# Performance work log

Measured on AMD Instinct MI355X. Metric: run time of the kernel, lower is better.

## Reference

```python
import jax, jax.numpy as jnp
import numpy as np

B, T, D, H, E = 4, 2048, 1024, 2048, 8
TOP_K = int(E * 0.25)  # = 2


def setup_inputs() -> dict:
    key = jax.random.key(0)
    ks = jax.random.split(key, 6)
    x = jax.random.normal(ks[0], (B, T, D), dtype=jnp.float32)
    gate = jax.random.normal(ks[1], (D, E), dtype=jnp.float32)
    # per-expert 2-layer MLP params (D -> H -> D), stacked over experts
    W1 = jax.random.normal(ks[2], (E, D, H), dtype=jnp.float32) * (D ** -0.5)
    b1 = jnp.zeros((E, H), dtype=jnp.float32)
    W2 = jax.random.normal(ks[3], (E, H, D), dtype=jnp.float32) * (H ** -0.5)
    b2 = jnp.zeros((E, D), dtype=jnp.float32)
    return {"x": x, "gate": gate, "W1": W1, "b1": b1, "W2": W2, "b2": b2}


def reference(x, gate, W1, b1, W2, b2):
    # gating: softmax over experts, then top-k mask, renormalize (L1 over experts)
    raw_gate = jax.nn.softmax(jnp.einsum('btd,de->bte', x, gate), axis=-1)  # [B,T,E]
    topk_scores, topk_idx = jax.lax.top_k(raw_gate, TOP_K)                   # [B,T,k]
    mask = jax.nn.one_hot(topk_idx, E, dtype=raw_gate.dtype).sum(axis=-2)    # [B,T,E]
    gate_topk = mask * raw_gate
    gate_topk = gate_topk / jnp.maximum(gate_topk.sum(axis=-1, keepdims=True), 1e-12)
    # dense all-expert compute (faithful to the original: every expert sees every token)
    h = jax.nn.relu(jnp.einsum('btd,edh->beth', x, W1) + b1[None, :, None, :])  # [B,E,T,H]
    expert_out = jnp.einsum('beth,ehd->betd', h, W2) + b2[None, :, None, :]     # [B,E,T,D]
    # weighted combine
    out = jnp.einsum('bte,betd->btd', gate_topk, expert_out)  # [B,T,D]
    return out
```

## Files before the change

### kernel.cpp

```cpp
#include <hip/hip_runtime.h>

#define E_      8
#define D_      1024
#define H_      2048
#define TOKENS  8192
#define RROWS   16384
#define HPAD_ROWS (RROWS + 128)

using bf16x8 = __attribute__((ext_vector_type(8))) __bf16;
using f32x4  = __attribute__((ext_vector_type(4))) float;

__device__ __forceinline__ unsigned short f2bf(float f) {
  unsigned u = __builtin_bit_cast(unsigned, f);
  u += 0x7fffu + ((u >> 16) & 1u);
  return (unsigned short)(u >> 16);
}
__device__ __forceinline__ float bf2f(unsigned short u) {
  unsigned v = (unsigned)u << 16;
  return __builtin_bit_cast(float, v);
}

#define GLDS16(g, l) __builtin_amdgcn_global_load_lds( \
    (const __attribute__((address_space(1))) unsigned int*)(g), \
    (__attribute__((address_space(3))) unsigned int*)(l), 16, 0, 0)

#define SBAR() asm volatile("s_barrier" ::: "memory")


__global__ void transpose_cvt2_kernel(const float* __restrict__ W1,
                                      unsigned short* __restrict__ w1t,
                                      const float* __restrict__ W2,
                                      unsigned short* __restrict__ w2t) {
  int b = blockIdx.x;
  const int nb1 = E_ * (D_ >> 6) * (H_ >> 6);
  const float* src; unsigned short* dst; int R, C;
  if (b < nb1) { src = W1; dst = w1t; R = D_; C = H_; }
  else         { src = W2; dst = w2t; R = H_; C = D_; b -= nb1; }
  int tilesC = C >> 6;
  int per = (R >> 6) * tilesC;
  int e = b / per, rem = b % per;
  int rb = rem / tilesC, cb = rem % tilesC;
  __shared__ float tile[64][65];
  const float* s = src + (size_t)e * R * C;
  unsigned short* d = dst + (size_t)e * R * C;
  int r0 = rb << 6, c0 = cb << 6;
#pragma unroll
  for (int i = 0; i < 16; i++) {
    int idx = threadIdx.x + i * 256;
    int lr = idx >> 6, lc = idx & 63;
    tile[lr][lc] = s[(size_t)(r0 + lr) * C + (c0 + lc)];
  }
  __syncthreads();
#pragma unroll
  for (int i = 0; i < 16; i++) {
    int idx = threadIdx.x + i * 256;
    int lr = idx >> 6, lc = idx & 63;
    d[(size_t)(c0 + lr) * R + (r0 + lc)] = f2bf(tile[lc][lr]);
  }
}

__global__ void gating_kernel(const float* __restrict__ x, const float* __restrict__ gate,
                              unsigned short* __restrict__ xb,
                              int* __restrict__ sel, float* __restrict__ wsel) {
  int lane = threadIdx.x & 63, wid = threadIdx.x >> 6;
  int t = (blockIdx.x << 2) + wid;
  const float* xr = x + (size_t)t * D_;
  unsigned short* xbr = xb + (size_t)t * D_;
  float acc[8];
#pragma unroll
  for (int e = 0; e < 8; e++) acc[e] = 0.f;
#pragma unroll
  for (int i = 0; i < 4; i++) {
    int d0 = (i << 8) + (lane << 2);
    float4 xv = *reinterpret_cast<const float4*>(xr + d0);
    ushort4 o = make_ushort4(f2bf(xv.x), f2bf(xv.y), f2bf(xv.z), f2bf(xv.w));
    *reinterpret_cast<ushort4*>(xbr + d0) = o;
    float xa[4] = {xv.x, xv.y, xv.z, xv.w};
#pragma unroll
    for (int j = 0; j < 4; j++) {
      const float4* g4 = reinterpret_cast<const float4*>(gate + (size_t)(d0 + j) * 8);
      float4 ga = g4[0], gb = g4[1];
      acc[0] += xa[j] * ga.x; acc[1] += xa[j] * ga.y;
      acc[2] += xa[j] * ga.z; acc[3] += xa[j] * ga.w;
      acc[4] += xa[j] * gb.x; acc[5] += xa[j] * gb.y;
      acc[6] += xa[j] * gb.z; acc[7] += xa[j] * gb.w;
    }
  }
#pragma unroll
  for (int e = 0; e < 8; e++) {
#pragma unroll
    for (int off = 32; off; off >>= 1) acc[e] += __shfl_xor(acc[e], off);
  }
  if (lane == 0) {
    int i0 = 0; float v0 = acc[0];
#pragma unroll
    for (int e = 1; e < 8; e++) if (acc[e] > v0) { v0 = acc[e]; i0 = e; }
    int i1 = -1; float v1 = -3.4e38f;
#pragma unroll
    for (int e = 0; e < 8; e++) if (e != i0 && acc[e] > v1) { v1 = acc[e]; i1 = e; }
    float p1 = expf(v1 - v0);
    float inv = 1.f / (1.f + p1);
    sel[t * 2] = i0; sel[t * 2 + 1] = i1;
    wsel[t * 2] = inv; wsel[t * 2 + 1] = p1 * inv;
  }
}

__global__ __launch_bounds__(1024) void route_kernel(
    const int* __restrict__ sel, int* __restrict__ cnt, int* __restrict__ off,
    int* __restrict__ tok_id, int* __restrict__ pos) {
  const int tid = threadIdx.x;
  const int lane = tid & 63, wid = tid >> 6;
  __shared__ int wtot[16][8];
  __shared__ int woff[16][8];
  __shared__ int offs[8];
  int sv[16];
  const int s0 = tid << 4;
#pragma unroll
  for (int q = 0; q < 4; q++) {
    int4 v = reinterpret_cast<const int4*>(sel + s0)[q];
    sv[q * 4 + 0] = v.x; sv[q * 4 + 1] = v.y;
    sv[q * 4 + 2] = v.z; sv[q * 4 + 3] = v.w;
  }
  int h[8];
#pragma unroll
  for (int e = 0; e < 8; e++) h[e] = 0;
#pragma unroll
  for (int j = 0; j < 16; j++) {
    int ev = sv[j];
#pragma unroll
    for (int e = 0; e < 8; e++) h[e] += (ev == e) ? 1 : 0;
  }
  int excl[8];
#pragma unroll
  for (int e = 0; e < 8; e++) {
    int v = h[e];
#pragma unroll
    for (int d = 1; d < 64; d <<= 1) {
      int u = __shfl_up(v, d);
      if (lane >= d) v += u;
    }
    excl[e] = v - h[e];
    if (lane == 63) wtot[wid][e] = v;
  }
  __syncthreads();
  if (tid == 0) {
    int run[8];
#pragma unroll
    for (int e = 0; e < 8; e++) run[e] = 0;
    for (int w = 0; w < 16; w++)
#pragma unroll
      for (int e = 0; e < 8; e++) { woff[w][e] = run[e]; run[e] += wtot[w][e]; }
    int a = 0;
    for (int e = 0; e < 8; e++) { offs[e] = a; off[e] = a; cnt[e] = run[e]; a += run[e]; }
  }
  __syncthreads();
  int base[8];
#pragma unroll
  for (int e = 0; e < 8; e++) base[e] = offs[e] + woff[wid][e] + excl[e];
#pragma unroll
  for (int j = 0; j < 16; j++) {
    int ev = sv[j];
    int p = 0;
#pragma unroll
    for (int e = 0; e < 8; e++) if (ev == e) { p = base[e]; base[e] = p + 1; }
    pos[s0 + j] = p;
    tok_id[p] = (s0 + j) >> 1;
  }
}


#define STAGE_A(slot, kh) do { \
  const size_t ko = (size_t)(kh) << 7; \
  _Pragma("unroll") \
  for (int i = 0; i < 4; i++) \
    GLDS16(Ab + gA[i] + ko, &Asm[slot][((wid << 2) + i) << 9]); \
} while (0)
#define STAGE_B(slot, kh) do { \
  const size_t ko = (size_t)(kh) << 7; \
  _Pragma("unroll") \
  for (int i = 0; i < 4; i++) \
    GLDS16(Bb + gB[i] + ko, &Bsm[slot][((wid << 2) + i) << 9]); \
} while (0)

__global__ __launch_bounds__(256, 2) void gemm1_kernel(
    const unsigned short* __restrict__ xb,
    const unsigned short* __restrict__ w1t,
    const float* __restrict__ b1,
    unsigned short* __restrict__ hbuf,
    const int* __restrict__ tok_id,
    const int* __restrict__ cnt, const int* __restrict__ off) {
  const int nwg = E_ * 64 * 16;
  const int raw = blockIdx.x;
  const int bid = (raw & 7) * (nwg >> 3) + (raw >> 3);
  const int e  = bid >> 10;
  const int rb = (bid >> 4) & 63;
  const int cb = bid & 15;
  const int rows = cnt[e];
  const int m0 = rb << 7;
  if (m0 >= rows) return;
  const int base = off[e];
  const int tid = threadIdx.x, lane = tid & 63, wid = tid >> 6;
  const int wr = wid >> 1, wc = wid & 1;

  __shared__ __align__(16) unsigned short Asm[2][128 * 64];
  __shared__ __align__(16) unsigned short Bsm[2][128 * 64];

  const int c8 = lane & 7, r8 = lane >> 3;
  const size_t swz = (size_t)((c8 ^ r8) << 4);
  size_t gA[4], gB[4];
  const int n0 = cb << 7;
#pragma unroll
  for (int i = 0; i < 4; i++) {
    int r = ((wid << 2) + i) << 3;
    int ar = m0 + r + r8; if (ar >= rows) ar = rows - 1;
    gA[i] = (size_t)tok_id[base + ar] * (D_ * 2) + swz;
    gB[i] = (size_t)(n0 + r + r8) * (D_ * 2) + swz;
  }
  const char* Ab = (const char*)xb;
  const char* Bb = (const char*)w1t + (size_t)e * H_ * D_ * 2;

  const int aRow = ((wr << 6) + (lane & 15)) * 128;
  const int bRow = ((wc << 6) + (lane & 15)) * 128;
  const int cby0 = (((lane >> 4)) ^ (lane & 7)) << 4;
  const int cby1 = ((4 + (lane >> 4)) ^ (lane & 7)) << 4;

  f32x4 acc[4][4] = {};
  const int KH = D_ / 64;

  STAGE_A(0, 0); STAGE_B(0, 0);
  STAGE_A(1, 1); STAGE_B(1, 1);
  asm volatile("s_waitcnt vmcnt(8)" ::: "memory");
  SBAR();

  for (int kh = 0; kh < KH; ++kh) {
    const int cur = kh & 1;
    const char* Ap = (const char*)&Asm[cur][0] + aRow;
    const char* Bp = (const char*)&Bsm[cur][0] + bRow;
    bf16x8 a[4], b[4], a2[4], b2[4];
#pragma unroll
    for (int m = 0; m < 4; m++) a[m]  = *(const bf16x8*)(Ap + cby0 + m * 2048);
#pragma unroll
    for (int n = 0; n < 4; n++) b[n]  = *(const bf16x8*)(Bp + cby0 + n * 2048);
#pragma unroll
    for (int m = 0; m < 4; m++) a2[m] = *(const bf16x8*)(Ap + cby1 + m * 2048);
#pragma unroll
    for (int n = 0; n < 4; n++) b2[n] = *(const bf16x8*)(Bp + cby1 + n * 2048);
    asm volatile("s_waitcnt lgkmcnt(0)" ::: "memory");
    __builtin_amdgcn_sched_barrier(0);
    SBAR();
    if (kh + 2 < KH) STAGE_A(cur, kh + 2);
    __builtin_amdgcn_s_setprio(1);
#pragma unroll
    for (int m = 0; m < 4; m++)
#pragma unroll
      for (int n = 0; n < 4; n++)
        acc[m][n] = __builtin_amdgcn_mfma_f32_16x16x32_bf16(a[m], b[n], acc[m][n], 0, 0, 0);
    __builtin_amdgcn_s_setprio(0);
    if (kh + 2 < KH) STAGE_B(cur, kh + 2);
    __builtin_amdgcn_s_setprio(1);
#pragma unroll
    for (int m = 0; m < 4; m++)
#pragma unroll
      for (int n = 0; n < 4; n++)
        acc[m][n] = __builtin_amdgcn_mfma_f32_16x16x32_bf16(a2[m], b2[n], acc[m][n], 0, 0, 0);
    __builtin_amdgcn_s_setprio(0);
    if (kh + 2 < KH) {
      asm volatile("s_waitcnt vmcnt(8)" ::: "memory");
    } else if (kh + 1 < KH) {
      asm volatile("s_waitcnt vmcnt(0)" ::: "memory");
    }
    SBAR();
  }

  const int rcnt = rows - m0;
  const float* b1e = b1 + e * H_;
#pragma unroll
  for (int m = 0; m < 4; m++) {
#pragma unroll
    for (int q = 0; q < 4; q++) {
      int rl = (wr << 6) + (m << 4) + ((lane >> 4) << 2) + q;
      if (rl < rcnt) {
        unsigned short* hrow = hbuf + (size_t)(base + m0 + rl) * H_;
#pragma unroll
        for (int n = 0; n < 4; n++) {
          int ncol = n0 + (wc << 6) + (n << 4) + (lane & 15);
          float v = acc[m][n][q] + b1e[ncol];
          hrow[ncol] = f2bf(fmaxf(v, 0.f));
        }
      }
    }
  }
}

__global__ __launch_bounds__(256, 2) void gemm2_kernel(
    const unsigned short* __restrict__ hbuf,
    const unsigned short* __restrict__ w2t,
    unsigned short* __restrict__ eout,
    const int* __restrict__ cnt, const int* __restrict__ off) {
  const int nwg = E_ * 64 * 8;
  const int raw = blockIdx.x;
  const int bid = (raw & 7) * (nwg >> 3) + (raw >> 3);
  const int e  = bid >> 9;
  const int rb = (bid >> 3) & 63;
  const int cb = bid & 7;
  const int rows = cnt[e];
  const int m0 = rb << 7;
  if (m0 >= rows) return;
  const int base = off[e];
  const int tid = threadIdx.x, lane = tid & 63, wid = tid >> 6;
  const int wr = wid >> 1, wc = wid & 1;

  __shared__ __align__(16) unsigned short Asm[2][128 * 64];
  __shared__ __align__(16) unsigned short Bsm[2][128 * 64];

  const int c8 = lane & 7, r8 = lane >> 3;
  const size_t swz = (size_t)((c8 ^ r8) << 4);
  size_t gA[4], gB[4];
  const int n0 = cb << 7;
#pragma unroll
  for (int i = 0; i < 4; i++) {
    int r = ((wid << 2) + i) << 3;
    gA[i] = (size_t)(base + m0 + r + r8) * (H_ * 2) + swz;
    gB[i] = (size_t)(n0 + r + r8) * (H_ * 2) + swz;
  }
  const char* Ab = (const char*)hbuf;
  const char* Bb = (const char*)w2t + (size_t)e * D_ * H_ * 2;

  const int aRow = ((wr << 6) + (lane & 15)) * 128;
  const int bRow = ((wc << 6) + (lane & 15)) * 128;
  const int cby0 = (((lane >> 4)) ^ (lane & 7)) << 4;
  const int cby1 = ((4 + (lane >> 4)) ^ (lane & 7)) << 4;

  f32x4 acc[4][4] = {};
  const int KH = H_ / 64;

  STAGE_A(0, 0); STAGE_B(0, 0);
  STAGE_A(1, 1); STAGE_B(1, 1);
  asm volatile("s_waitcnt vmcnt(8)" ::: "memory");
  SBAR();

  for (int kh = 0; kh < KH; ++kh) {
    const int cur = kh & 1;
    const char* Ap = (const char*)&Asm[cur][0] + aRow;
    const char* Bp = (const char*)&Bsm[cur][0] + bRow;
    bf16x8 a[4], b[4], a2[4], b2[4];
#pragma unroll
    for (int m = 0; m < 4; m++) a[m]  = *(const bf16x8*)(Ap + cby0 + m * 2048);
#pragma unroll
    for (int n = 0; n < 4; n++) b[n]  = *(const bf16x8*)(Bp + cby0 + n * 2048);
#pragma unroll
    for (int m = 0; m < 4; m++) a2[m] = *(const bf16x8*)(Ap + cby1 + m * 2048);
#pragma unroll
    for (int n = 0; n < 4; n++) b2[n] = *(const bf16x8*)(Bp + cby1 + n * 2048);
    asm volatile("s_waitcnt lgkmcnt(0)" ::: "memory");
    __builtin_amdgcn_sched_barrier(0);
    SBAR();
    if (kh + 2 < KH) STAGE_A(cur, kh + 2);
    __builtin_amdgcn_s_setprio(1);
#pragma unroll
    for (int m = 0; m < 4; m++)
#pragma unroll
      for (int n = 0; n < 4; n++)
        acc[m][n] = __builtin_amdgcn_mfma_f32_16x16x32_bf16(a[m], b[n], acc[m][n], 0, 0, 0);
    __builtin_amdgcn_s_setprio(0);
    if (kh + 2 < KH) STAGE_B(cur, kh + 2);
    __builtin_amdgcn_s_setprio(1);
#pragma unroll
    for (int m = 0; m < 4; m++)
#pragma unroll
      for (int n = 0; n < 4; n++)
        acc[m][n] = __builtin_amdgcn_mfma_f32_16x16x32_bf16(a2[m], b2[n], acc[m][n], 0, 0, 0);
    __builtin_amdgcn_s_setprio(0);
    if (kh + 2 < KH) {
      asm volatile("s_waitcnt vmcnt(8)" ::: "memory");
    } else if (kh + 1 < KH) {
      asm volatile("s_waitcnt vmcnt(0)" ::: "memory");
    }
    SBAR();
  }

  const int rcnt = rows - m0;
#pragma unroll
  for (int m = 0; m < 4; m++) {
#pragma unroll
    for (int q = 0; q < 4; q++) {
      int rl = (wr << 6) + (m << 4) + ((lane >> 4) << 2) + q;
      if (rl < rcnt) {
        unsigned short* erow = eout + (size_t)(base + m0 + rl) * D_;
#pragma unroll
        for (int n = 0; n < 4; n++) {
          int ncol = n0 + (wc << 6) + (n << 4) + (lane & 15);
          erow[ncol] = f2bf(acc[m][n][q]);
        }
      }
    }
  }
}

__global__ void combine_kernel(const unsigned short* __restrict__ eout,
                               const float* __restrict__ b2,
                               const int* __restrict__ sel, const float* __restrict__ wsel,
                               const int* __restrict__ pos,
                               float* __restrict__ out) {
  int t = (blockIdx.x << 2) + (threadIdx.x >> 6);
  int lane = threadIdx.x & 63;
  int e0 = sel[t * 2], e1 = sel[t * 2 + 1];
  float w0 = wsel[t * 2], w1 = wsel[t * 2 + 1];
  int p0 = pos[t * 2], p1 = pos[t * 2 + 1];
  const unsigned short* y0r = eout + (size_t)p0 * D_;
  const unsigned short* y1r = eout + (size_t)p1 * D_;
  const float* c0r = b2 + (size_t)e0 * D_;
  const float* c1r = b2 + (size_t)e1 * D_;
  float* orow = out + (size_t)t * D_;
#pragma unroll
  for (int j = 0; j < 4; j++) {
    int d = (j << 8) + (lane << 2);
    ushort4 y0 = *reinterpret_cast<const ushort4*>(y0r + d);
    ushort4 y1 = *reinterpret_cast<const ushort4*>(y1r + d);
    float4 c0 = *reinterpret_cast<const float4*>(c0r + d);
    float4 c1 = *reinterpret_cast<const float4*>(c1r + d);
    float4 o;
    o.x = w0 * (bf2f(y0.x) + c0.x) + w1 * (bf2f(y1.x) + c1.x);
    o.y = w0 * (bf2f(y0.y) + c0.y) + w1 * (bf2f(y1.y) + c1.y);
    o.z = w0 * (bf2f(y0.z) + c0.z) + w1 * (bf2f(y1.z) + c1.z);
    o.w = w0 * (bf2f(y0.w) + c0.w) + w1 * (bf2f(y1.w) + c1.w);
    *reinterpret_cast<float4*>(orow + d) = o;
  }
}


extern "C" void kernel_launch(void* const* d_in, const int* in_sizes, int n_in,
                              void* d_out, int out_size, void* d_ws, size_t ws_size,
                              hipStream_t stream) {
  (void)in_sizes; (void)n_in; (void)ws_size; (void)out_size;
  const float* x    = (const float*)d_in[0];
  const float* gate = (const float*)d_in[1];
  const float* W1   = (const float*)d_in[2];
  const float* b1   = (const float*)d_in[3];
  const float* W2   = (const float*)d_in[4];
  const float* b2   = (const float*)d_in[5];
  float* out = (float*)d_out;

  char* p = (char*)d_ws;
  unsigned short* xb   = (unsigned short*)p; p += (size_t)TOKENS * D_ * 2;
  unsigned short* w1t  = (unsigned short*)p; p += (size_t)E_ * H_ * D_ * 2;
  unsigned short* w2t  = (unsigned short*)p; p += (size_t)E_ * D_ * H_ * 2;
  unsigned short* hbuf = (unsigned short*)p; p += (size_t)HPAD_ROWS * H_ * 2;
  int*   tok  = (int*)p;   p += (size_t)RROWS * 4;
  int*   pos  = (int*)p;   p += (size_t)TOKENS * 2 * 4;
  int*   sel  = (int*)p;   p += (size_t)TOKENS * 2 * 4;
  float* wsel = (float*)p; p += (size_t)TOKENS * 2 * 4;
  int* cnt    = (int*)p;   p += 32 * 4;
  int* off    = (int*)p;   p += 32 * 4;
  unsigned short* eout = w1t;

  const int nb1 = E_ * (D_ / 64) * (H_ / 64);
  const int nb2 = E_ * (H_ / 64) * (D_ / 64);
  transpose_cvt2_kernel<<<nb1 + nb2, 256, 0, stream>>>(W1, w1t, W2, w2t);
  gating_kernel<<<TOKENS / 4, 256, 0, stream>>>(x, gate, xb, sel, wsel);
  route_kernel<<<1, 1024, 0, stream>>>(sel, cnt, off, tok, pos);
  gemm1_kernel<<<E_ * 64 * 16, 256, 0, stream>>>(xb, w1t, b1, hbuf, tok, cnt, off);
  gemm2_kernel<<<E_ * 64 * 8, 256, 0, stream>>>(hbuf, w2t, eout, cnt, off);
  combine_kernel<<<TOKENS / 4, 256, 0, stream>>>(eout, b2, sel, wsel, pos, out);
}
```

Before: 295.1 us.

## Fuse gating into transpose prologue and widen gemm1 tile to 128x256 with 512 threads

Merges the gating kernel and the weight transpose/convert kernel into one launch, so one kernel boundary goes away and the two independent stages can run at the same time. Rewrites gemm1 to use 8 waves per workgroup, each block covering 128 rows by 256 columns of H. The wider tile means the gathered A rows are reused across twice as many columns. The cost is one workgroup per CU (launch bounds 512,1), which lowers occupancy, and the MFMA chains are merged without the interleaved B staging.

After: 297.1 us. No clear change (+0.7%).

```diff
diff --git a/kernel.cpp b/kernel.cpp
--- a/kernel.cpp
+++ b/kernel.cpp
@@ -27,11 +27,59 @@
 #define SBAR() asm volatile("s_barrier" ::: "memory")
 
 
-__global__ void transpose_cvt2_kernel(const float* __restrict__ W1,
-                                      unsigned short* __restrict__ w1t,
-                                      const float* __restrict__ W2,
-                                      unsigned short* __restrict__ w2t) {
+__global__ void prologue_kernel(const float* __restrict__ x, const float* __restrict__ gate,
+                                unsigned short* __restrict__ xb,
+                                int* __restrict__ sel, float* __restrict__ wsel,
+                                const float* __restrict__ W1, unsigned short* __restrict__ w1t,
+                                const float* __restrict__ W2, unsigned short* __restrict__ w2t) {
+  __shared__ float tile[64][65];
   int b = blockIdx.x;
+  const int NG = TOKENS / 4;
+  if (b < NG) {
+    int lane = threadIdx.x & 63, wid = threadIdx.x >> 6;
+    int t = (b << 2) + wid;
+    const float* xr = x + (size_t)t * D_;
+    unsigned short* xbr = xb + (size_t)t * D_;
+    float acc[8];
+#pragma unroll
+    for (int e = 0; e < 8; e++) acc[e] = 0.f;
+#pragma unroll
+    for (int i = 0; i < 4; i++) {
+      int d0 = (i << 8) + (lane << 2);
+      float4 xv = *reinterpret_cast<const float4*>(xr + d0);
+      ushort4 o = make_ushort4(f2bf(xv.x), f2bf(xv.y), f2bf(xv.z), f2bf(xv.w));
+      *reinterpret_cast<ushort4*>(xbr + d0) = o;
+      float xa[4] = {xv.x, xv.y, xv.z, xv.w};
+#pragma unroll
+      for (int j = 0; j < 4; j++) {
+        const float4* g4 = reinterpret_cast<const float4*>(gate + (size_t)(d0 + j) * 8);
+        float4 ga = g4[0], gb = g4[1];
+        acc[0] += xa[j] * ga.x; acc[1] += xa[j] * ga.y;
+        acc[2] += xa[j] * ga.z; acc[3] += xa[j] * ga.w;
+        acc[4] += xa[j] * gb.x; acc[5] += xa[j] * gb.y;
+        acc[6] += xa[j] * gb.z; acc[7] += xa[j] * gb.w;
+      }
+    }
+#pragma unroll
+    for (int e = 0; e < 8; e++) {
+#pragma unroll
+      for (int off = 32; off; off >>= 1) acc[e] += __shfl_xor(acc[e], off);
+    }
+    if (lane == 0) {
+      int i0 = 0; float v0 = acc[0];
+#pragma unroll
+      for (int e = 1; e < 8; e++) if (acc[e] > v0) { v0 = acc[e]; i0 = e; }
+      int i1 = -1; float v1 = -3.4e38f;
+#pragma unroll
+      for (int e = 0; e < 8; e++) if (e != i0 && acc[e] > v1) { v1 = acc[e]; i1 = e; }
+      float p1 = expf(v1 - v0);
+      float inv = 1.f / (1.f + p1);
+      sel[t * 2] = i0; sel[t * 2 + 1] = i1;
+      wsel[t * 2] = inv; wsel[t * 2 + 1] = p1 * inv;
+    }
+    return;
+  }
+  b -= NG;
   const int nb1 = E_ * (D_ >> 6) * (H_ >> 6);
   const float* src; unsigned short* dst; int R, C;
   if (b < nb1) { src = W1; dst = w1t; R = D_; C = H_; }
@@ -40,7 +88,6 @@
   int per = (R >> 6) * tilesC;
   int e = b / per, rem = b % per;
   int rb = rem / tilesC, cb = rem % tilesC;
-  __shared__ float tile[64][65];
   const float* s = src + (size_t)e * R * C;
   unsigned short* d = dst + (size_t)e * R * C;
   int r0 = rb << 6, c0 = cb << 6;
@@ -56,52 +103,6 @@
     int idx = threadIdx.x + i * 256;
     int lr = idx >> 6, lc = idx & 63;
     d[(size_t)(c0 + lr) * R + (r0 + lc)] = f2bf(tile[lc][lr]);
-  }
-}
-
-__global__ void gating_kernel(const float* __restrict__ x, const float* __restrict__ gate,
-                              unsigned short* __restrict__ xb,
-                              int* __restrict__ sel, float* __restrict__ wsel) {
-  int lane = threadIdx.x & 63, wid = threadIdx.x >> 6;
-  int t = (blockIdx.x << 2) + wid;
-  const float* xr = x + (size_t)t * D_;
-  unsigned short* xbr = xb + (size_t)t * D_;
-  float acc[8];
-#pragma unroll
-  for (int e = 0; e < 8; e++) acc[e] = 0.f;
-#pragma unroll
-  for (int i = 0; i < 4; i++) {
-    int d0 = (i << 8) + (lane << 2);
-    float4 xv = *reinterpret_cast<const float4*>(xr + d0);
-    ushort4 o = make_ushort4(f2bf(xv.x), f2bf(xv.y), f2bf(xv.z), f2bf(xv.w));
-    *reinterpret_cast<ushort4*>(xbr + d0) = o;
-    float xa[4] = {xv.x, xv.y, xv.z, xv.w};
-#pragma unroll
-    for (int j = 0; j < 4; j++) {
-      const float4* g4 = reinterpret_cast<const float4*>(gate + (size_t)(d0 + j) * 8);
-      float4 ga = g4[0], gb = g4[1];
-      acc[0] += xa[j] * ga.x; acc[1] += xa[j] * ga.y;
-      acc[2] += xa[j] * ga.z; acc[3] += xa[j] * ga.w;
-      acc[4] += xa[j] * gb.x; acc[5] += xa[j] * gb.y;
-      acc[6] += xa[j] * gb.z; acc[7] += xa[j] * gb.w;
-    }
-  }
-#pragma unroll
-  for (int e = 0; e < 8; e++) {
-#pragma unroll
-    for (int off = 32; off; off >>= 1) acc[e] += __shfl_xor(acc[e], off);
-  }
-  if (lane == 0) {
-    int i0 = 0; float v0 = acc[0];
-#pragma unroll
-    for (int e = 1; e < 8; e++) if (acc[e] > v0) { v0 = acc[e]; i0 = e; }
-    int i1 = -1; float v1 = -3.4e38f;
-#pragma unroll
-    for (int e = 0; e < 8; e++) if (e != i0 && acc[e] > v1) { v1 = acc[e]; i1 = e; }
-    float p1 = expf(v1 - v0);
-    float inv = 1.f / (1.f + p1);
-    sel[t * 2] = i0; sel[t * 2 + 1] = i1;
-    wsel[t * 2] = inv; wsel[t * 2 + 1] = p1 * inv;
   }
 }
 
@@ -168,6 +169,126 @@
   }
 }
 
+
+#define STAGE1(slot, kh) do { \
+  const size_t ko = (size_t)(kh) << 7; \
+  _Pragma("unroll") \
+  for (int i = 0; i < 2; i++) \
+    GLDS16(Ab + gA[i] + ko, &Asm[slot][((wid << 1) + i) << 9]); \
+  _Pragma("unroll") \
+  for (int i = 0; i < 4; i++) \
+    GLDS16(Bb + gB[i] + ko, &Bsm[slot][((wid << 2) + i) << 9]); \
+} while (0)
+
+__global__ __launch_bounds__(512, 1) void gemm1_kernel(
+    const unsigned short* __restrict__ xb,
+    const unsigned short* __restrict__ w1t,
+    const float* __restrict__ b1,
+    unsigned short* __restrict__ hbuf,
+    const int* __restrict__ tok_id,
+    const int* __restrict__ cnt, const int* __restrict__ off) {
+  const int nwg = E_ * 64 * 8;
+  const int raw = blockIdx.x;
+  const int bid = (raw & 7) * (nwg >> 3) + (raw >> 3);
+  const int e  = bid >> 9;
+  const int rb = (bid >> 3) & 63;
+  const int cb = bid & 7;
+  const int rows = cnt[e];
+  const int m0 = rb << 7;
+  if (m0 >= rows) return;
+  const int base = off[e];
+  const int tid = threadIdx.x, lane = tid & 63, wid = tid >> 6;
+  const int wr = wid >> 2, wc = wid & 3;
+
+  __shared__ __align__(16) unsigned short Asm[2][128 * 64];
+  __shared__ __align__(16) unsigned short Bsm[2][256 * 64];
+
+  const size_t swz = (size_t)(((lane & 7) ^ (lane >> 3)) << 4);
+  size_t gA[2], gB[4];
+  const int n0 = cb << 8;
+#pragma unroll
+  for (int i = 0; i < 2; i++) {
+    int r = (((wid << 1) + i) << 3) + (lane >> 3);
+    int ar = m0 + r; if (ar >= rows) ar = rows - 1;
+    gA[i] = (size_t)tok_id[base + ar] * (D_ * 2) + swz;
+  }
+#pragma unroll
+  for (int i = 0; i < 4; i++) {
+    int r = (((wid << 2) + i) << 3) + (lane >> 3);
+    gB[i] = (size_t)(n0 + r) * (D_ * 2) + swz;
+  }
+  const char* Ab = (const char*)xb;
+  const char* Bb = (const char*)w1t + (size_t)e * H_ * D_ * 2;
+
+  const int aRow = ((wr << 6) + (lane & 15)) * 128;
+  const int bRow = ((wc << 6) + (lane & 15)) * 128;
+  const int cby0 = (((lane >> 4)) ^ (lane & 7)) << 4;
+  const int cby1 = ((4 + (lane >> 4)) ^ (lane & 7)) << 4;
+
+  f32x4 acc[4][4] = {};
+  const int KH = D_ / 64;
+
+  STAGE1(0, 0);
+  STAGE1(1, 1);
+  asm volatile("s_waitcnt vmcnt(6)" ::: "memory");
+  SBAR();
+
+  for (int kh = 0; kh < KH; ++kh) {
+    const int cur = kh & 1;
+    const char* Ap = (const char*)&Asm[cur][0] + aRow;
+    const char* Bp = (const char*)&Bsm[cur][0] + bRow;
+    bf16x8 a[4], b[4], a2[4], b2[4];
+#pragma unroll
+    for (int m = 0; m < 4; m++) a[m]  = *(const bf16x8*)(Ap + cby0 + m * 2048);
+#pragma unroll
+    for (int n = 0; n < 4; n++) b[n]  = *(const bf16x8*)(Bp + cby0 + n * 2048);
+#pragma unroll
+    for (int m = 0; m < 4; m++) a2[m] = *(const bf16x8*)(Ap + cby1 + m * 2048);
+#pragma unroll
+    for (int n = 0; n < 4; n++) b2[n] = *(const bf16x8*)(Bp + cby1 + n * 2048);
+    asm volatile("s_waitcnt lgkmcnt(0)" ::: "memory");
+    __builtin_amdgcn_sched_barrier(0);
+    SBAR();
+    if (kh + 2 < KH) STAGE1(cur, kh + 2);
+    __builtin_amdgcn_s_setprio(1);
+#pragma unroll
+    for (int m = 0; m < 4; m++)
+#pragma unroll
+      for (int n = 0; n < 4; n++)
+        acc[m][n] = __builtin_amdgcn_mfma_f32_16x16x32_bf16(a[m], b[n], acc[m][n], 0, 0, 0);
+#pragma unroll
+    for (int m = 0; m < 4; m++)
+#pragma unroll
+      for (int n = 0; n < 4; n++)
+        acc[m][n] = __builtin_amdgcn_mfma_f32_16x16x32_bf16(a2[m], b2[n], acc[m][n], 0, 0, 0);
+    __builtin_amdgcn_s_setprio(0);
+    if (kh + 2 < KH) {
+      asm volatile("s_waitcnt vmcnt(6)" ::: "memory");
+    } else if (kh + 1 < KH) {
+      asm volatile("s_waitcnt vmcnt(0)" ::: "memory");
+    }
+    SBAR();
+  }
+
+  const int rcnt = rows - m0;
+  const float* b1e = b1 + e * H_;
+#pragma unroll
+  for (int m = 0; m < 4; m++) {
+#pragma unroll
+    for (int q = 0; q < 4; q++) {
+      int rl = (wr << 6) + (m << 4) + ((lane >> 4) << 2) + q;
+      if (rl < rcnt) {
+        unsigned short* hrow = hbuf + (size_t)(base + m0 + rl) * H_;
+#pragma unroll
+        for (int n = 0; n < 4; n++) {
+          int ncol = n0 + (wc << 6) + (n << 4) + (lane & 15);
+          float v = acc[m][n][q] + b1e[ncol];
+          hrow[ncol] = f2bf(fmaxf(v, 0.f));
+        }
+      }
+    }
+  }
+}
 
 #define STAGE_A(slot, kh) do { \
   const size_t ko = (size_t)(kh) << 7; \
@@ -181,116 +302,6 @@
   for (int i = 0; i < 4; i++) \
     GLDS16(Bb + gB[i] + ko, &Bsm[slot][((wid << 2) + i) << 9]); \
 } while (0)
-
-__global__ __launch_bounds__(256, 2) void gemm1_kernel(
-    const unsigned short* __restrict__ xb,
-    const unsigned short* __restrict__ w1t,
-    const float* __restrict__ b1,
-    unsigned short* __restrict__ hbuf,
-    const int* __restrict__ tok_id,
-    const int* __restrict__ cnt, const int* __restrict__ off) {
-  const int nwg = E_ * 64 * 16;
-  const int raw = blockIdx.x;
-  const int bid = (raw & 7) * (nwg >> 3) + (raw >> 3);
-  const int e  = bid >> 10;
-  const int rb = (bid >> 4) & 63;
-  const int cb = bid & 15;
-  const int rows = cnt[e];
-  const int m0 = rb << 7;
-  if (m0 >= rows) return;
-  const int base = off[e];
-  const int tid = threadIdx.x, lane = tid & 63, wid = tid >> 6;
-  const int wr = wid >> 1, wc = wid & 1;
-
-  __shared__ __align__(16) unsigned short Asm[2][128 * 64];
-  __shared__ __align__(16) unsigned short Bsm[2][128 * 64];
-
-  const int c8 = lane & 7, r8 = lane >> 3;
-  const size_t swz = (size_t)((c8 ^ r8) << 4);
-  size_t gA[4], gB[4];
-  const int n0 = cb << 7;
-#pragma unroll
-  for (int i = 0; i < 4; i++) {
-    int r = ((wid << 2) + i) << 3;
-    int ar = m0 + r + r8; if (ar >= rows) ar = rows - 1;
-    gA[i] = (size_t)tok_id[base + ar] * (D_ * 2) + swz;
-    gB[i] = (size_t)(n0 + r + r8) * (D_ * 2) + swz;
-  }
-  const char* Ab = (const char*)xb;
-  const char* Bb = (const char*)w1t + (size_t)e * H_ * D_ * 2;
-
-  const int aRow = ((wr << 6) + (lane & 15)) * 128;
-  const int bRow = ((wc << 6) + (lane & 15)) * 128;
-  const int cby0 = (((lane >> 4)) ^ (lane & 7)) << 4;
-  const int cby1 = ((4 + (lane >> 4)) ^ (lane & 7)) << 4;
-
-  f32x4 acc[4][4] = {};
-  const int KH = D_ / 64;
-
-  STAGE_A(0, 0); STAGE_B(0, 0);
-  STAGE_A(1, 1); STAGE_B(1, 1);
-  asm volatile("s_waitcnt vmcnt(8)" ::: "memory");
-  SBAR();
-
-  for (int kh = 0; kh < KH; ++kh) {
-    const int cur = kh & 1;
-    const char* Ap = (const char*)&Asm[cur][0] + aRow;
-    const char* Bp = (const char*)&Bsm[cur][0] + bRow;
-    bf16x8 a[4], b[4], a2[4], b2[4];
-#pragma unroll
-    for (int m = 0; m < 4; m++) a[m]  = *(const bf16x8*)(Ap + cby0 + m * 2048);
-#pragma unroll
-    for (int n = 0; n < 4; n++) b[n]  = *(const bf16x8*)(Bp + cby0 + n * 2048);
-#pragma unroll
-    for (int m = 0; m < 4; m++) a2[m] = *(const bf16x8*)(Ap + cby1 + m * 2048);
-#pragma unroll
-    for (int n = 0; n < 4; n++) b2[n] = *(const bf16x8*)(Bp + cby1 + n * 2048);
-    asm volatile("s_waitcnt lgkmcnt(0)" ::: "memory");
-    __builtin_amdgcn_sched_barrier(0);
-    SBAR();
-    if (kh + 2 < KH) STAGE_A(cur, kh + 2);
-    __builtin_amdgcn_s_setprio(1);
-#pragma unroll
-    for (int m = 0; m < 4; m++)
-#pragma unroll
-      for (int n = 0; n < 4; n++)
-        acc[m][n] = __builtin_amdgcn_mfma_f32_16x16x32_bf16(a[m], b[n], acc[m][n], 0, 0, 0);
-    __builtin_amdgcn_s_setprio(0);
-    if (kh + 2 < KH) STAGE_B(cur, kh + 2);
-    __builtin_amdgcn_s_setprio(1);
-#pragma unroll
-    for (int m = 0; m < 4; m++)
-#pragma unroll
-      for (int n = 0; n < 4; n++)
-        acc[m][n] = __builtin_amdgcn_mfma_f32_16x16x32_bf16(a2[m], b2[n], acc[m][n], 0, 0, 0);
-    __builtin_amdgcn_s_setprio(0);
-    if (kh + 2 < KH) {
-      asm volatile("s_waitcnt vmcnt(8)" ::: "memory");
-    } else if (kh + 1 < KH) {
-      asm volatile("s_waitcnt vmcnt(0)" ::: "memory");
-    }
-    SBAR();
-  }
-
-  const int rcnt = rows - m0;
-  const float* b1e = b1 + e * H_;
-#pragma unroll
-  for (int m = 0; m < 4; m++) {
-#pragma unroll
-    for (int q = 0; q < 4; q++) {
-      int rl = (wr << 6) + (m << 4) + ((lane >> 4) << 2) + q;
-      if (rl < rcnt) {
-        unsigned short* hrow = hbuf + (size_t)(base + m0 + rl) * H_;
-#pragma unroll
-        for (int n = 0; n < 4; n++) {
-          int ncol = n0 + (wc << 6) + (n << 4) + (lane & 15);
-          float v = acc[m][n][q] + b1e[ncol];
-          hrow[ncol] = f2bf(fmaxf(v, 0.f));
-        }
-      }
-    }
-  }
-}
 
 __global__ __launch_bounds__(256, 2) void gemm2_kernel(
     const unsigned short* __restrict__ hbuf,
@@ -456,10 +467,10 @@
 
   const int nb1 = E_ * (D_ / 64) * (H_ / 64);
   const int nb2 = E_ * (H_ / 64) * (D_ / 64);
-  transpose_cvt2_kernel<<<nb1 + nb2, 256, 0, stream>>>(W1, w1t, W2, w2t);
-  gating_kernel<<<TOKENS / 4, 256, 0, stream>>>(x, gate, xb, sel, wsel);
+  prologue_kernel<<<TOKENS / 4 + nb1 + nb2, 256, 0, stream>>>(
+      x, gate, xb, sel, wsel, W1, w1t, W2, w2t);
   route_kernel<<<1, 1024, 0, stream>>>(sel, cnt, off, tok, pos);
-  gemm1_kernel<<<E_ * 64 * 16, 256, 0, stream>>>(xb, w1t, b1, hbuf, tok, cnt, off);
+  gemm1_kernel<<<E_ * 64 * 8, 512, 0, stream>>>(xb, w1t, b1, hbuf, tok, cnt, off);
   gemm2_kernel<<<E_ * 64 * 8, 256, 0, stream>>>(hbuf, w2t, eout, cnt, off);
   combine_kernel<<<TOKENS / 4, 256, 0, stream>>>(eout, b2, sel, wsel, pos, out);
 }
```
